# Optimization experiments

Measured on AMD Instinct MI355X. Metric: run time of the kernel, lower is better.

## Reference

```python
import jax, jax.numpy as jnp
import numpy as np

B, S, H = 2, 2048, 2048
INTER = 1024
N_ROUTED = 8
ZERO = 4
TOTAL = N_ROUTED + ZERO
TOP_K = 2
SCALE = 1.5


def setup_inputs() -> dict:
    key = jax.random.key(0)
    k0, k1, k2, k3, k4, k5 = jax.random.split(key, 6)
    w = 0.02  # weight init scale
    return {
        "hidden_states": jax.random.normal(k0, (B, S, H), jnp.float32),
        "classifier_w": jax.random.normal(k1, (TOTAL, H), jnp.float32) * w,
        "e_score_correction_bias": jax.random.normal(k2, (TOTAL,), jnp.float32) * w,
        "gate_w": jax.random.normal(k3, (N_ROUTED, INTER, H), jnp.float32) * w,
        "up_w": jax.random.normal(k4, (N_ROUTED, INTER, H), jnp.float32) * w,
        "down_w": jax.random.normal(k5, (N_ROUTED, H, INTER), jnp.float32) * w,
    }


def reference(hidden_states, classifier_w, e_score_correction_bias, gate_w, up_w, down_w):
    x = hidden_states  # [B,S,H]
    total = classifier_w.shape[0]
    n_routed = gate_w.shape[0]

    # --- Router: softmax over all experts, bias only for selection ---
    logits = jnp.einsum('bsh,eh->bse', x, classifier_w)          # [B,S,total]
    probs = jax.nn.softmax(logits, axis=-1)
    biased = probs + e_score_correction_bias
    _, idx = jax.lax.top_k(biased, TOP_K)                         # [B,S,K] int
    rw = jnp.take_along_axis(probs, idx, axis=-1) * SCALE         # unbiased probs as weights

    # Dense per-expert weight via one-hot combine (Equal+Mul+ReduceSum in original)
    w_full = jnp.sum(jax.nn.one_hot(idx, total, dtype=x.dtype) * rw[..., None], axis=-2)  # [B,S,total]

    # --- Compute ALL routed experts densely (matches original op graph) ---
    g = jnp.einsum('bsh,eih->bsei', x, gate_w)                    # [B,S,E,INTER]
    u = jnp.einsum('bsh,eih->bsei', x, up_w)
    act = jax.nn.silu(g) * u
    expert_out = jnp.einsum('bsei,ehi->bseh', act, down_w)        # [B,S,E,H]

    out = jnp.einsum('bse,bseh->bsh', w_full[..., :n_routed], expert_out)
    # Zero (identity) experts pass hidden_states through
    out = out + x * jnp.sum(w_full[..., n_routed:], axis=-1, keepdims=True)
    return out
```

## Files before the change

kernel.cpp:

```cpp
#include <hip/hip_runtime.h>
#include <cstdint>

#define T_TOKENS 4096
#define HDIM 2048
#define IDIM 1024
#define NEXP 8
#define NTOT 12
#define MAX_SLOTS 8320

typedef __bf16 bf16x8_t __attribute__((ext_vector_type(8)));
typedef float f32x4_t __attribute__((ext_vector_type(4)));
typedef unsigned short u16x8_t __attribute__((ext_vector_type(8)));
typedef unsigned short u16x4_t __attribute__((ext_vector_type(4)));

__device__ __forceinline__ unsigned short f2bf(float f) {
    unsigned int u = __builtin_bit_cast(unsigned int, f);
    u += 0x7fffu + ((u >> 16) & 1u);
    return (unsigned short)(u >> 16);
}
__device__ __forceinline__ float bfu2f(unsigned short u) {
    unsigned int v = ((unsigned int)u) << 16;
    return __builtin_bit_cast(float, v);
}
__device__ __forceinline__ void async16(const unsigned short* g, unsigned short* l) {
    __builtin_amdgcn_global_load_lds(
        (const unsigned int __attribute__((address_space(1)))*)g,
        (unsigned int __attribute__((address_space(3)))*)l,
        16, 0, 0);
}
__device__ __forceinline__ void cvt16(const float* src, unsigned short* dst) {
    f32x4_t f0 = ((const f32x4_t*)src)[0];
    f32x4_t f1 = ((const f32x4_t*)src)[1];
    f32x4_t f2 = ((const f32x4_t*)src)[2];
    f32x4_t f3 = ((const f32x4_t*)src)[3];
    u16x8_t a, b;
#pragma unroll
    for (int j = 0; j < 4; ++j) { a[j] = f2bf(f0[j]); a[4 + j] = f2bf(f1[j]); }
#pragma unroll
    for (int j = 0; j < 4; ++j) { b[j] = f2bf(f2[j]); b[4 + j] = f2bf(f3[j]); }
    ((u16x8_t*)dst)[0] = a;
    ((u16x8_t*)dst)[1] = b;
}

__global__ void init_kernel(int* __restrict__ meta) {
    int i = threadIdx.x;
    if (i < 32) meta[i] = 0;
}

__global__ void noop_kernel() {}

__global__ void cvtbf_kernel(const float* __restrict__ s, unsigned short* __restrict__ d, int n8) {
    int stride = gridDim.x * blockDim.x;
    for (int i = blockIdx.x * blockDim.x + threadIdx.x; i < n8; i += stride) {
        const f32x4_t* p = (const f32x4_t*)(s + (size_t)i * 8);
        f32x4_t a = p[0], b = p[1];
        u16x8_t o;
#pragma unroll
        for (int j = 0; j < 4; ++j) { o[j] = f2bf(a[j]); o[4 + j] = f2bf(b[j]); }
        ((u16x8_t*)d)[i] = o;
    }
}

__global__ void router_kernel(const float* __restrict__ x,
                              const float* __restrict__ cw,
                              const float* __restrict__ bias,
                              int* __restrict__ counts,
                              int* __restrict__ tok_e,
                              float* __restrict__ tok_w,
                              float* __restrict__ zero_w,
                              unsigned short* __restrict__ xb) {
    const int token = blockIdx.x;
    const int ln = threadIdx.x;
    const float* xr = x + (size_t)token * HDIM;
    float acc[NTOT];
#pragma unroll
    for (int e = 0; e < NTOT; ++e) acc[e] = 0.f;
    for (int h0 = ln * 4; h0 < HDIM; h0 += 256) {
        f32x4_t xv = *(const f32x4_t*)(xr + h0);
        if (xb) {
            u16x4_t o;
#pragma unroll
            for (int j = 0; j < 4; ++j) o[j] = f2bf(xv[j]);
            *(u16x4_t*)(xb + (size_t)token * HDIM + h0) = o;
        }
#pragma unroll
        for (int e = 0; e < NTOT; ++e) {
            f32x4_t wv = *(const f32x4_t*)(cw + e * HDIM + h0);
            acc[e] += xv[0] * wv[0] + xv[1] * wv[1] + xv[2] * wv[2] + xv[3] * wv[3];
        }
    }
#pragma unroll
    for (int e = 0; e < NTOT; ++e) {
        float v = acc[e];
#pragma unroll
        for (int s = 32; s > 0; s >>= 1) v += __shfl_xor(v, s, 64);
        acc[e] = v;
    }
    if (ln == 0) {
        float mx = acc[0];
#pragma unroll
        for (int e = 1; e < NTOT; ++e) mx = fmaxf(mx, acc[e]);
        float p[NTOT];
        float sum = 0.f;
#pragma unroll
        for (int e = 0; e < NTOT; ++e) { p[e] = __expf(acc[e] - mx); sum += p[e]; }
        float inv = 1.f / sum;
#pragma unroll
        for (int e = 0; e < NTOT; ++e) p[e] *= inv;
        float b[NTOT];
#pragma unroll
        for (int e = 0; e < NTOT; ++e) b[e] = p[e] + bias[e];
        int i0 = 0; float v0 = b[0];
#pragma unroll
        for (int e = 1; e < NTOT; ++e) if (b[e] > v0) { v0 = b[e]; i0 = e; }
        int i1 = -1; float v1 = -3.0e38f;
#pragma unroll
        for (int e = 0; e < NTOT; ++e) if (e != i0 && b[e] > v1) { v1 = b[e]; i1 = e; }
        if (i1 < 0) i1 = (i0 == 0) ? 1 : 0;
        float w0 = p[i0] * 1.5f, w1 = p[i1] * 1.5f;
        tok_e[2 * token] = i0; tok_e[2 * token + 1] = i1;
        tok_w[2 * token] = w0; tok_w[2 * token + 1] = w1;
        float zw = 0.f;
        if (i0 >= NEXP) zw += w0; else atomicAdd(&counts[i0], 1);
        if (i1 >= NEXP) zw += w1; else atomicAdd(&counts[i1], 1);
        zero_w[token] = zw;
    }
}

__global__ void scan_kernel(const int* __restrict__ counts, int* __restrict__ offs) {
    if (threadIdx.x == 0 && blockIdx.x == 0) {
        int a = 0;
        for (int e = 0; e < NEXP; ++e) {
            offs[e] = a;
            int c = counts[e];
            if (c < 0) c = 0;
            if (c > T_TOKENS) c = T_TOKENS;
            a += c;
        }
        if (a > 2 * T_TOKENS) a = 2 * T_TOKENS;
        offs[NEXP] = a;
    }
}

__global__ void place_kernel(const int* __restrict__ tok_e, const float* __restrict__ tok_w,
                             const int* __restrict__ offs, int* __restrict__ fill,
                             int* __restrict__ token_list, float* __restrict__ slot_w,
                             int* __restrict__ map) {
    int token = blockIdx.x * blockDim.x + threadIdx.x;
    if (token >= T_TOKENS) return;
#pragma unroll
    for (int j = 0; j < 2; ++j) {
        int e = tok_e[2 * token + j];
        int m = -1;
        if (e >= 0 && e < NEXP) {
            int pos = atomicAdd(&fill[e], 1);
            int slot = offs[e] + pos;
            if (slot >= 0 && slot < 2 * T_TOKENS) {
                token_list[slot] = token;
                slot_w[slot] = tok_w[2 * token + j];
                m = slot;
            }
        }
        map[2 * token + j] = m;
    }
}

__launch_bounds__(256, 3)
__global__ void gemm1_kernel(const unsigned short* __restrict__ xb,
                             const unsigned short* __restrict__ gwb,
                             const unsigned short* __restrict__ uwb,
                             const int* __restrict__ offs,
                             const int* __restrict__ token_list,
                             const float* __restrict__ slot_w,
                             unsigned short* __restrict__ act) {
    const int e = blockIdx.z;
    const int off = offs[e];
    int Me = offs[e + 1] - off;
    if (Me < 0) Me = 0;
    if (Me > T_TOKENS) Me = T_TOKENS;
    const int m0 = blockIdx.y * 64;
    if (m0 >= Me) return;
    const int n0 = blockIdx.x * 128;

    __shared__ __align__(16) unsigned short As[64][32];
    __shared__ __align__(16) unsigned short Gs[128][32];
    __shared__ __align__(16) unsigned short Us[128][32];

    const int tid = threadIdx.x;
    const int wv = tid >> 6, ln = tid & 63;

    int tr = m0 + wv * 16 + (ln >> 2);
    if (tr >= Me) tr = Me - 1;
    int tok = token_list[off + tr];
    if (tok < 0 || tok >= T_TOKENS) tok = 0;
    const unsigned short* aA = xb + (size_t)tok * HDIM + (ln & 3) * 8;
    unsigned short* lA = &As[wv * 16][0];

    const size_t wrow = (size_t)(n0 + wv * 32 + (ln >> 2)) * HDIM + (ln & 3) * 8;
    const unsigned short* aG0 = gwb + (size_t)e * IDIM * HDIM + wrow;
    const unsigned short* aG1 = aG0 + (size_t)16 * HDIM;
    const unsigned short* aU0 = uwb + (size_t)e * IDIM * HDIM + wrow;
    const unsigned short* aU1 = aU0 + (size_t)16 * HDIM;
    unsigned short* lG0 = &Gs[wv * 32][0];
    unsigned short* lG1 = &Gs[wv * 32 + 16][0];
    unsigned short* lU0 = &Us[wv * 32][0];
    unsigned short* lU1 = &Us[wv * 32 + 16][0];

    const int wm = wv & 1, wn = wv >> 1;
    const int fr = ln & 15;
    const int fk = (ln >> 4) * 8;

    f32x4_t accg[2][4] = {};
    f32x4_t accu[2][4] = {};

    for (int k0 = 0; k0 < HDIM; k0 += 32) {
        async16(aA + k0, lA);
        async16(aG0 + k0, lG0);
        async16(aG1 + k0, lG1);
        async16(aU0 + k0, lU0);
        async16(aU1 + k0, lU1);
        __syncthreads();
        bf16x8_t af[2], gf[4], uf[4];
#pragma unroll
        for (int t = 0; t < 2; ++t)
            af[t] = *(const bf16x8_t*)&As[wm * 32 + t * 16 + fr][fk];
#pragma unroll
        for (int t = 0; t < 4; ++t) {
            gf[t] = *(const bf16x8_t*)&Gs[wn * 64 + t * 16 + fr][fk];
            uf[t] = *(const bf16x8_t*)&Us[wn * 64 + t * 16 + fr][fk];
        }
#pragma unroll
        for (int mt = 0; mt < 2; ++mt)
#pragma unroll
            for (int nt = 0; nt < 4; ++nt) {
                accg[mt][nt] = __builtin_amdgcn_mfma_f32_16x16x32_bf16(af[mt], gf[nt], accg[mt][nt], 0, 0, 0);
                accu[mt][nt] = __builtin_amdgcn_mfma_f32_16x16x32_bf16(af[mt], uf[nt], accu[mt][nt], 0, 0, 0);
            }
        __syncthreads();
    }

#pragma unroll
    for (int mt = 0; mt < 2; ++mt) {
#pragma unroll
        for (int r = 0; r < 4; ++r) {
            int rloc = wm * 32 + mt * 16 + (ln >> 4) * 4 + r;
            int grow = m0 + rloc;
            if (grow < Me) {
                float w = slot_w[off + grow];
                size_t rb = (size_t)(off + grow) * IDIM + n0;
#pragma unroll
                for (int nt = 0; nt < 4; ++nt) {
                    float g = accg[mt][nt][r];
                    float u = accu[mt][nt][r];
                    float s = g / (1.f + __expf(-g));
                    act[rb + wn * 64 + nt * 16 + fr] = f2bf(s * u * w);
                }
            }
        }
    }
}

__launch_bounds__(256, 3)
__global__ void gemm2_kernel(const unsigned short* __restrict__ act,
                             const unsigned short* __restrict__ dwb,
                             const int* __restrict__ offs,
                             unsigned short* __restrict__ dout) {
    const int e = blockIdx.z;
    const int off = offs[e];
    int Me = offs[e + 1] - off;
    if (Me < 0) Me = 0;
    if (Me > T_TOKENS) Me = T_TOKENS;
    const int m0 = blockIdx.y * 128;
    if (m0 >= Me) return;
    const int n0 = blockIdx.x * 128;

    __shared__ __align__(16) unsigned short As[128][32];
    __shared__ __align__(16) unsigned short Bs[128][32];

    const int tid = threadIdx.x;
    const int wv = tid >> 6, ln = tid & 63;
    const int sc = (ln & 3) * 8;

    const int sr = wv * 16 + (ln >> 2);
    int ar0 = off + m0 + sr;      if (ar0 >= MAX_SLOTS) ar0 = MAX_SLOTS - 1;
    int ar1 = off + m0 + 64 + sr; if (ar1 >= MAX_SLOTS) ar1 = MAX_SLOTS - 1;
    const unsigned short* aA0 = act + (size_t)ar0 * IDIM + sc;
    const unsigned short* aA1 = act + (size_t)ar1 * IDIM + sc;
    unsigned short* lA0 = &As[wv * 16][0];
    unsigned short* lA1 = &As[64 + wv * 16][0];

    const unsigned short* aB0 = dwb + (size_t)e * HDIM * IDIM +
                                (size_t)(n0 + wv * 32 + (ln >> 2)) * IDIM + sc;
    const unsigned short* aB1 = aB0 + (size_t)16 * IDIM;
    unsigned short* lB0 = &Bs[wv * 32][0];
    unsigned short* lB1 = &Bs[wv * 32 + 16][0];

    const int wm = wv & 1, wn = wv >> 1;
    const int fr = ln & 15;
    const int fk = (ln >> 4) * 8;

    f32x4_t acc[4][4] = {};

    for (int k0 = 0; k0 < IDIM; k0 += 32) {
        async16(aA0 + k0, lA0);
        async16(aA1 + k0, lA1);
        async16(aB0 + k0, lB0);
        async16(aB1 + k0, lB1);
        __syncthreads();
        bf16x8_t af[4], bfr[4];
#pragma unroll
        for (int t = 0; t < 4; ++t) {
            af[t] = *(const bf16x8_t*)&As[wm * 64 + t * 16 + fr][fk];
            bfr[t] = *(const bf16x8_t*)&Bs[wn * 64 + t * 16 + fr][fk];
        }
#pragma unroll
        for (int mt = 0; mt < 4; ++mt)
#pragma unroll
            for (int nt = 0; nt < 4; ++nt)
                acc[mt][nt] = __builtin_amdgcn_mfma_f32_16x16x32_bf16(af[mt], bfr[nt], acc[mt][nt], 0, 0, 0);
        __syncthreads();
    }

#pragma unroll
    for (int mt = 0; mt < 4; ++mt) {
#pragma unroll
        for (int r = 0; r < 4; ++r) {
            int rloc = wm * 64 + mt * 16 + (ln >> 4) * 4 + r;
            int grow = m0 + rloc;
            if (grow < Me) {
                size_t rb = (size_t)(off + grow) * HDIM + n0;
#pragma unroll
                for (int nt = 0; nt < 4; ++nt)
                    dout[rb + wn * 64 + nt * 16 + fr] = f2bf(acc[mt][nt][r]);
            }
        }
    }
}

__launch_bounds__(256, 2)
__global__ void gemm1_fb(const float* __restrict__ x,
                         const float* __restrict__ gate_w,
                         const float* __restrict__ up_w,
                         const int* __restrict__ offs,
                         const int* __restrict__ token_list,
                         const float* __restrict__ slot_w,
                         unsigned short* __restrict__ act) {
    const int e = blockIdx.z;
    const int off = offs[e];
    int Me = offs[e + 1] - off;
    if (Me < 0) Me = 0;
    if (Me > T_TOKENS) Me = T_TOKENS;
    const int m0 = blockIdx.y * 128;
    if (m0 >= Me) return;
    const int n0 = blockIdx.x * 128;

    __shared__ __align__(16) unsigned short As[128][32];
    __shared__ __align__(16) unsigned short Gs[128][32];
    __shared__ __align__(16) unsigned short Us[128][32];

    const int tid = threadIdx.x;
    const int srow = tid >> 1;
    const int shalf = (tid & 1) * 16;

    int tr = m0 + srow; if (tr >= Me) tr = Me - 1;
    int tok = token_list[off + tr];
    if (tok < 0 || tok >= T_TOKENS) tok = 0;
    const float* aA = x + (size_t)tok * HDIM + shalf;
    const float* aG = gate_w + (size_t)e * IDIM * HDIM + (size_t)(n0 + srow) * HDIM + shalf;
    const float* aU = up_w + (size_t)e * IDIM * HDIM + (size_t)(n0 + srow) * HDIM + shalf;
    unsigned short* lA = &As[srow][shalf];
    unsigned short* lG = &Gs[srow][shalf];
    unsigned short* lU = &Us[srow][shalf];

    const int wv = tid >> 6, ln = tid & 63;
    const int wm = wv & 1, wn = wv >> 1;
    const int fr = ln & 15;
    const int fk = (ln >> 4) * 8;

    f32x4_t accg[4][4] = {};
    f32x4_t accu[4][4] = {};

    for (int k0 = 0; k0 < HDIM; k0 += 32) {
        cvt16(aA + k0, lA);
        cvt16(aG + k0, lG);
        cvt16(aU + k0, lU);
        __syncthreads();
        bf16x8_t af[4], gf[4], uf[4];
#pragma unroll
        for (int t = 0; t < 4; ++t) {
            af[t] = *(const bf16x8_t*)&As[wm * 64 + t * 16 + fr][fk];
            gf[t] = *(const bf16x8_t*)&Gs[wn * 64 + t * 16 + fr][fk];
            uf[t] = *(const bf16x8_t*)&Us[wn * 64 + t * 16 + fr][fk];
        }
#pragma unroll
        for (int mt = 0; mt < 4; ++mt)
#pragma unroll
            for (int nt = 0; nt < 4; ++nt) {
                accg[mt][nt] = __builtin_amdgcn_mfma_f32_16x16x32_bf16(af[mt], gf[nt], accg[mt][nt], 0, 0, 0);
                accu[mt][nt] = __builtin_amdgcn_mfma_f32_16x16x32_bf16(af[mt], uf[nt], accu[mt][nt], 0, 0, 0);
            }
        __syncthreads();
    }

#pragma unroll
    for (int mt = 0; mt < 4; ++mt) {
#pragma unroll
        for (int r = 0; r < 4; ++r) {
            int rloc = wm * 64 + mt * 16 + (ln >> 4) * 4 + r;
            int grow = m0 + rloc;
            if (grow < Me) {
                float w = slot_w[off + grow];
                size_t rb = (size_t)(off + grow) * IDIM + n0;
#pragma unroll
                for (int nt = 0; nt < 4; ++nt) {
                    float g = accg[mt][nt][r];
                    float u = accu[mt][nt][r];
                    float s = g / (1.f + __expf(-g));
                    act[rb + wn * 64 + nt * 16 + fr] = f2bf(s * u * w);
                }
            }
        }
    }
}

__launch_bounds__(256, 2)
__global__ void gemm2_fb(const unsigned short* __restrict__ act,
                         const float* __restrict__ dwn,
                         const int* __restrict__ offs,
                         unsigned short* __restrict__ dout) {
    const int e = blockIdx.z;
    const int off = offs[e];
    int Me = offs[e + 1] - off;
    if (Me < 0) Me = 0;
    if (Me > T_TOKENS) Me = T_TOKENS;
    const int m0 = blockIdx.y * 128;
    if (m0 >= Me) return;
    const int n0 = blockIdx.x * 128;

    __shared__ __align__(16) unsigned short As[128][32];
    __shared__ __align__(16) unsigned short Bs[128][32];

    const int tid = threadIdx.x;
    const int wv = tid >> 6, ln = tid & 63;

    const int sr0 = wv * 16 + (ln >> 2);
    const int sc = (ln & 3) * 8;
    int ar0 = off + m0 + sr0;      if (ar0 >= MAX_SLOTS) ar0 = MAX_SLOTS - 1;
    int ar1 = off + m0 + 64 + sr0; if (ar1 >= MAX_SLOTS) ar1 = MAX_SLOTS - 1;
    const unsigned short* aA0 = act + (size_t)ar0 * IDIM + sc;
    const unsigned short* aA1 = act + (size_t)ar1 * IDIM + sc;
    unsigned short* lA0 = &As[wv * 16][0];
    unsigned short* lA1 = &As[64 + wv * 16][0];

    const int srow = tid >> 1;
    const int shalf = (tid & 1) * 16;
    const float* aB = dwn + (size_t)e * HDIM * IDIM + (size_t)(n0 + srow) * IDIM + shalf;
    unsigned short* lB = &Bs[srow][shalf];

    const int wm = wv & 1, wn = wv >> 1;
    const int fr = ln & 15;
    const int fk = (ln >> 4) * 8;

    f32x4_t acc[4][4] = {};

    for (int k0 = 0; k0 < IDIM; k0 += 32) {
        async16(aA0 + k0, lA0);
        async16(aA1 + k0, lA1);
        cvt16(aB + k0, lB);
        __syncthreads();
        bf16x8_t af[4], bfr[4];
#pragma unroll
        for (int t = 0; t < 4; ++t) {
            af[t] = *(const bf16x8_t*)&As[wm * 64 + t * 16 + fr][fk];
            bfr[t] = *(const bf16x8_t*)&Bs[wn * 64 + t * 16 + fr][fk];
        }
#pragma unroll
        for (int mt = 0; mt < 4; ++mt)
#pragma unroll
            for (int nt = 0; nt < 4; ++nt)
                acc[mt][nt] = __builtin_amdgcn_mfma_f32_16x16x32_bf16(af[mt], bfr[nt], acc[mt][nt], 0, 0, 0);
        __syncthreads();
    }

#pragma unroll
    for (int mt = 0; mt < 4; ++mt) {
#pragma unroll
        for (int r = 0; r < 4; ++r) {
            int rloc = wm * 64 + mt * 16 + (ln >> 4) * 4 + r;
            int grow = m0 + rloc;
            if (grow < Me) {
                size_t rb = (size_t)(off + grow) * HDIM + n0;
#pragma unroll
                for (int nt = 0; nt < 4; ++nt)
                    dout[rb + wn * 64 + nt * 16 + fr] = f2bf(acc[mt][nt][r]);
            }
        }
    }
}

__global__ void finalize_kernel(const float* __restrict__ x,
                                const unsigned short* __restrict__ dout,
                                const int* __restrict__ map,
                                const float* __restrict__ zero_w,
                                float* __restrict__ out) {
    int gid = blockIdx.x * blockDim.x + threadIdx.x;
    int token = gid >> 8;
    int hg = (gid & 255) * 8;
    int s0 = map[2 * token], s1 = map[2 * token + 1];
    float zw = zero_w[token];
    size_t base = (size_t)token * HDIM + hg;
    f32x4_t x0 = *(const f32x4_t*)(x + base);
    f32x4_t x1 = *(const f32x4_t*)(x + base + 4);
    float o[8];
#pragma unroll
    for (int j = 0; j < 4; ++j) { o[j] = zw * x0[j]; o[4 + j] = zw * x1[j]; }
    if (s0 >= 0 && s0 < 2 * T_TOKENS) {
        u16x8_t d = *(const u16x8_t*)(dout + (size_t)s0 * HDIM + hg);
#pragma unroll
        for (int j = 0; j < 8; ++j) o[j] += bfu2f(d[j]);
    }
    if (s1 >= 0 && s1 < 2 * T_TOKENS) {
        u16x8_t d = *(const u16x8_t*)(dout + (size_t)s1 * HDIM + hg);
#pragma unroll
        for (int j = 0; j < 8; ++j) o[j] += bfu2f(d[j]);
    }
    f32x4_t o0, o1;
#pragma unroll
    for (int j = 0; j < 4; ++j) { o0[j] = o[j]; o1[j] = o[4 + j]; }
    *(f32x4_t*)(out + base) = o0;
    *(f32x4_t*)(out + base + 4) = o1;
}

extern "C" void kernel_launch(void* const* d_in, const int* in_sizes, int n_in,
                              void* d_out, int out_size, void* d_ws, size_t ws_size,
                              hipStream_t stream) {
    const float* x = (const float*)d_in[0];
    const float* cw = (const float*)d_in[1];
    const float* bias = (const float*)d_in[2];
    const float* gw = (const float*)d_in[3];
    const float* uw = (const float*)d_in[4];
    const float* dw = (const float*)d_in[5];
    float* out = (float*)d_out;

    char* ws = (char*)d_ws;
    int* counts = (int*)(ws + 0);
    int* fill = (int*)(ws + 32);
    int* offs = (int*)(ws + 64);
    int* tok_e = (int*)(ws + 128);
    float* tok_w = (float*)(ws + 32896);
    float* zero_w = (float*)(ws + 65664);
    int* map = (int*)(ws + 82048);
    int* token_list = (int*)(ws + 114816);
    float* slot_w = (float*)(ws + 148096);
    unsigned short* act = (unsigned short*)(ws + 181504);
    unsigned short* dout = (unsigned short*)(ws + 17220864);
    const size_t needed_small = 51299584ull;
    unsigned short* xb  = (unsigned short*)(ws + 51299584ull);
    unsigned short* gwb = (unsigned short*)(ws + 68076800ull);
    unsigned short* uwb = (unsigned short*)(ws + 101631232ull);
    unsigned short* dwb = (unsigned short*)(ws + 135185664ull);
    const size_t needed_big = 168740096ull;

    if (ws_size < needed_small) {
        noop_kernel<<<1, 64, 0, stream>>>();
        return;
    }

    init_kernel<<<1, 64, 0, stream>>>((int*)ws);

    if (ws_size >= needed_big) {
        router_kernel<<<T_TOKENS, 64, 0, stream>>>(x, cw, bias, counts, tok_e, tok_w, zero_w, xb);
        scan_kernel<<<1, 64, 0, stream>>>(counts, offs);
        place_kernel<<<(T_TOKENS + 255) / 256, 256, 0, stream>>>(tok_e, tok_w, offs, fill,
                                                                 token_list, slot_w, map);
        const int n8w = NEXP * IDIM * HDIM / 8;
        cvtbf_kernel<<<2048, 256, 0, stream>>>(gw, gwb, n8w);
        cvtbf_kernel<<<2048, 256, 0, stream>>>(uw, uwb, n8w);
        cvtbf_kernel<<<2048, 256, 0, stream>>>(dw, dwb, n8w);
        gemm1_kernel<<<dim3(IDIM / 128, 64, NEXP), 256, 0, stream>>>(xb, gwb, uwb, offs,
                                                                     token_list, slot_w, act);
        gemm2_kernel<<<dim3(HDIM / 128, 32, NEXP), 256, 0, stream>>>(act, dwb, offs, dout);
    } else {
        router_kernel<<<T_TOKENS, 64, 0, stream>>>(x, cw, bias, counts, tok_e, tok_w, zero_w,
                                                   (unsigned short*)nullptr);
        scan_kernel<<<1, 64, 0, stream>>>(counts, offs);
        place_kernel<<<(T_TOKENS + 255) / 256, 256, 0, stream>>>(tok_e, tok_w, offs, fill,
                                                                 token_list, slot_w, map);
        gemm1_fb<<<dim3(IDIM / 128, 32, NEXP), 256, 0, stream>>>(x, gw, uw, offs,
                                                                 token_list, slot_w, act);
        gemm2_fb<<<dim3(HDIM / 128, 32, NEXP), 256, 0, stream>>>(act, dw, offs, dout);
    }

    finalize_kernel<<<(T_TOKENS * HDIM / 8 + 255) / 256, 256, 0, stream>>>(x, dout, map,
                                                                           zero_w, out);
}
```

Baseline: 531.8 us.

## Interleave gate/up weights into one packed matrix and use 128x128 gemm1 tiles

Gate and up weights are converted to bf16 into one interleaved buffer: each 32-row block holds 16 gate rows followed by 16 up rows. This lets gemm1 run as a single 128x128 tile GEMM whose adjacent accumulator tiles pair gate with up for the SiLU epilogue. The three conversion kernels are merged into one launch, and the gemm2 B-tile row mapping is changed to contiguous 16-row chunks per wave. The aim is more MMA work per loaded A tile and fewer launches, at the cost of a scattered read pattern in the pack kernel and a larger accumulator register footprint in gemm1.

```diff
diff --git a/kernel.cpp b/kernel.cpp
--- a/kernel.cpp
+++ b/kernel.cpp
@@ -49,15 +49,37 @@
 
 __global__ void noop_kernel() {}
 
-__global__ void cvtbf_kernel(const float* __restrict__ s, unsigned short* __restrict__ d, int n8) {
+__global__ void pack_w_kernel(const float* __restrict__ gw, const float* __restrict__ uw,
+                              const float* __restrict__ dw,
+                              unsigned short* __restrict__ guwb,
+                              unsigned short* __restrict__ dwb) {
+    const int n8_gu = NEXP * 2 * IDIM * HDIM / 8;
+    const int n8_d = NEXP * HDIM * IDIM / 8;
     int stride = gridDim.x * blockDim.x;
-    for (int i = blockIdx.x * blockDim.x + threadIdx.x; i < n8; i += stride) {
-        const f32x4_t* p = (const f32x4_t*)(s + (size_t)i * 8);
-        f32x4_t a = p[0], b = p[1];
-        u16x8_t o;
-#pragma unroll
-        for (int j = 0; j < 4; ++j) { o[j] = f2bf(a[j]); o[4 + j] = f2bf(b[j]); }
-        ((u16x8_t*)d)[i] = o;
+    for (int i = blockIdx.x * blockDim.x + threadIdx.x; i < n8_gu + n8_d; i += stride) {
+        if (i < n8_gu) {
+            size_t f = (size_t)i * 8;
+            int h = (int)(f & (HDIM - 1));
+            int p = (int)((f >> 11) & 2047);
+            int e = (int)(f >> 22);
+            int j = p >> 5, r = p & 31;
+            const float* base = (r < 16) ? gw : uw;
+            const float* src = base + ((size_t)e * IDIM + 16 * j + (r & 15)) * HDIM + h;
+            f32x4_t a = ((const f32x4_t*)src)[0];
+            f32x4_t b = ((const f32x4_t*)src)[1];
+            u16x8_t o;
+#pragma unroll
+            for (int q = 0; q < 4; ++q) { o[q] = f2bf(a[q]); o[4 + q] = f2bf(b[q]); }
+            ((u16x8_t*)guwb)[i] = o;
+        } else {
+            int k = i - n8_gu;
+            const f32x4_t* p4 = (const f32x4_t*)(dw + (size_t)k * 8);
+            f32x4_t a = p4[0], b = p4[1];
+            u16x8_t o;
+#pragma unroll
+            for (int q = 0; q < 4; ++q) { o[q] = f2bf(a[q]); o[4 + q] = f2bf(b[q]); }
+            ((u16x8_t*)dwb)[k] = o;
+        }
     }
 }
 
@@ -167,8 +189,7 @@
 
 __launch_bounds__(256, 3)
 __global__ void gemm1_kernel(const unsigned short* __restrict__ xb,
-                             const unsigned short* __restrict__ gwb,
-                             const unsigned short* __restrict__ uwb,
+                             const unsigned short* __restrict__ guwb,
                              const int* __restrict__ offs,
                              const int* __restrict__ token_list,
                              const float* __restrict__ slot_w,
@@ -178,82 +199,74 @@
     int Me = offs[e + 1] - off;
     if (Me < 0) Me = 0;
     if (Me > T_TOKENS) Me = T_TOKENS;
-    const int m0 = blockIdx.y * 64;
+    const int m0 = blockIdx.y * 128;
     if (m0 >= Me) return;
     const int n0 = blockIdx.x * 128;
 
-    __shared__ __align__(16) unsigned short As[64][32];
-    __shared__ __align__(16) unsigned short Gs[128][32];
-    __shared__ __align__(16) unsigned short Us[128][32];
+    __shared__ __align__(16) unsigned short As[128][32];
+    __shared__ __align__(16) unsigned short Bs[128][32];
 
     const int tid = threadIdx.x;
     const int wv = tid >> 6, ln = tid & 63;
-
-    int tr = m0 + wv * 16 + (ln >> 2);
-    if (tr >= Me) tr = Me - 1;
-    int tok = token_list[off + tr];
-    if (tok < 0 || tok >= T_TOKENS) tok = 0;
-    const unsigned short* aA = xb + (size_t)tok * HDIM + (ln & 3) * 8;
-    unsigned short* lA = &As[wv * 16][0];
-
-    const size_t wrow = (size_t)(n0 + wv * 32 + (ln >> 2)) * HDIM + (ln & 3) * 8;
-    const unsigned short* aG0 = gwb + (size_t)e * IDIM * HDIM + wrow;
-    const unsigned short* aG1 = aG0 + (size_t)16 * HDIM;
-    const unsigned short* aU0 = uwb + (size_t)e * IDIM * HDIM + wrow;
-    const unsigned short* aU1 = aU0 + (size_t)16 * HDIM;
-    unsigned short* lG0 = &Gs[wv * 32][0];
-    unsigned short* lG1 = &Gs[wv * 32 + 16][0];
-    unsigned short* lU0 = &Us[wv * 32][0];
-    unsigned short* lU1 = &Us[wv * 32 + 16][0];
+    const int sc = (ln & 3) * 8;
+
+    int tr0 = m0 + wv * 16 + (ln >> 2);      if (tr0 >= Me) tr0 = Me - 1;
+    int tr1 = m0 + 64 + wv * 16 + (ln >> 2); if (tr1 >= Me) tr1 = Me - 1;
+    int tok0 = token_list[off + tr0]; if (tok0 < 0 || tok0 >= T_TOKENS) tok0 = 0;
+    int tok1 = token_list[off + tr1]; if (tok1 < 0 || tok1 >= T_TOKENS) tok1 = 0;
+    const unsigned short* aA0 = xb + (size_t)tok0 * HDIM + sc;
+    const unsigned short* aA1 = xb + (size_t)tok1 * HDIM + sc;
+    unsigned short* lA0 = &As[wv * 16][0];
+    unsigned short* lA1 = &As[64 + wv * 16][0];
+
+    const unsigned short* aB0 = guwb + (size_t)e * 2 * IDIM * HDIM +
+                                (size_t)(n0 + wv * 16 + (ln >> 2)) * HDIM + sc;
+    const unsigned short* aB1 = aB0 + (size_t)64 * HDIM;
+    unsigned short* lB0 = &Bs[wv * 16][0];
+    unsigned short* lB1 = &Bs[64 + wv * 16][0];
 
     const int wm = wv & 1, wn = wv >> 1;
     const int fr = ln & 15;
     const int fk = (ln >> 4) * 8;
 
-    f32x4_t accg[2][4] = {};
-    f32x4_t accu[2][4] = {};
+    f32x4_t acc[4][4] = {};
 
     for (int k0 = 0; k0 < HDIM; k0 += 32) {
-        async16(aA + k0, lA);
-        async16(aG0 + k0, lG0);
-        async16(aG1 + k0, lG1);
-        async16(aU0 + k0, lU0);
-        async16(aU1 + k0, lU1);
-        __syncthreads();
-        bf16x8_t af[2], gf[4], uf[4];
-#pragma unroll
-        for (int t = 0; t < 2; ++t)
-            af[t] = *(const bf16x8_t*)&As[wm * 32 + t * 16 + fr][fk];
+        async16(aA0 + k0, lA0);
+        async16(aA1 + k0, lA1);
+        async16(aB0 + k0, lB0);
+        async16(aB1 + k0, lB1);
+        __syncthreads();
+        bf16x8_t af[4], bfr[4];
 #pragma unroll
         for (int t = 0; t < 4; ++t) {
-            gf[t] = *(const bf16x8_t*)&Gs[wn * 64 + t * 16 + fr][fk];
-            uf[t] = *(const bf16x8_t*)&Us[wn * 64 + t * 16 + fr][fk];
-        }
-#pragma unroll
-        for (int mt = 0; mt < 2; ++mt)
-#pragma unroll
-            for (int nt = 0; nt < 4; ++nt) {
-                accg[mt][nt] = __builtin_amdgcn_mfma_f32_16x16x32_bf16(af[mt], gf[nt], accg[mt][nt], 0, 0, 0);
-                accu[mt][nt] = __builtin_amdgcn_mfma_f32_16x16x32_bf16(af[mt], uf[nt], accu[mt][nt], 0, 0, 0);
-            }
-        __syncthreads();
-    }
-
-#pragma unroll
-    for (int mt = 0; mt < 2; ++mt) {
+            af[t] = *(const bf16x8_t*)&As[wm * 64 + t * 16 + fr][fk];
+            bfr[t] = *(const bf16x8_t*)&Bs[wn * 64 + t * 16 + fr][fk];
+        }
+#pragma unroll
+        for (int mt = 0; mt < 4; ++mt)
+#pragma unroll
+            for (int nt = 0; nt < 4; ++nt)
+                acc[mt][nt] = __builtin_amdgcn_mfma_f32_16x16x32_bf16(af[mt], bfr[nt], acc[mt][nt], 0, 0, 0);
+        __syncthreads();
+    }
+
+    const int ibase = (n0 >> 1) + wn * 32;
+#pragma unroll
+    for (int mt = 0; mt < 4; ++mt) {
 #pragma unroll
         for (int r = 0; r < 4; ++r) {
-            int rloc = wm * 32 + mt * 16 + (ln >> 4) * 4 + r;
+            int rloc = wm * 64 + mt * 16 + (ln >> 4) * 4 + r;
             int grow = m0 + rloc;
             if (grow < Me) {
                 float w = slot_w[off + grow];
-                size_t rb = (size_t)(off + grow) * IDIM + n0;
-#pragma unroll
-                for (int nt = 0; nt < 4; ++nt) {
-                    float g = accg[mt][nt][r];
-                    float u = accu[mt][nt][r];
+                size_t rb = (size_t)(off + grow) * IDIM + ibase;
+#pragma unroll
+                for (int t = 0; t < 2; ++t) {
+                    float g = acc[mt][2 * t][r];
+                    float u = acc[mt][2 * t + 1][r];
                     float s = g / (1.f + __expf(-g));
-                    act[rb + wn * 64 + nt * 16 + fr] = f2bf(s * u * w);
+                    act[rb + t * 16 + fr] = f2bf(s * u * w);
                 }
             }
         }
@@ -290,10 +303,10 @@
     unsigned short* lA1 = &As[64 + wv * 16][0];
 
     const unsigned short* aB0 = dwb + (size_t)e * HDIM * IDIM +
-                                (size_t)(n0 + wv * 32 + (ln >> 2)) * IDIM + sc;
-    const unsigned short* aB1 = aB0 + (size_t)16 * IDIM;
-    unsigned short* lB0 = &Bs[wv * 32][0];
-    unsigned short* lB1 = &Bs[wv * 32 + 16][0];
+                                (size_t)(n0 + wv * 16 + (ln >> 2)) * IDIM + sc;
+    const unsigned short* aB1 = aB0 + (size_t)64 * IDIM;
+    unsigned short* lB0 = &Bs[wv * 16][0];
+    unsigned short* lB1 = &Bs[64 + wv * 16][0];
 
     const int wm = wv & 1, wn = wv >> 1;
     const int fr = ln & 15;
@@ -555,10 +568,9 @@
     unsigned short* act = (unsigned short*)(ws + 181504);
     unsigned short* dout = (unsigned short*)(ws + 17220864);
     const size_t needed_small = 51299584ull;
-    unsigned short* xb  = (unsigned short*)(ws + 51299584ull);
-    unsigned short* gwb = (unsigned short*)(ws + 68076800ull);
-    unsigned short* uwb = (unsigned short*)(ws + 101631232ull);
-    unsigned short* dwb = (unsigned short*)(ws + 135185664ull);
+    unsigned short* xb   = (unsigned short*)(ws + 51299584ull);
+    unsigned short* guwb = (unsigned short*)(ws + 68076800ull);
+    unsigned short* dwb  = (unsigned short*)(ws + 135185664ull);
     const size_t needed_big = 168740096ull;
 
     if (ws_size < needed_small) {
@@ -573,12 +585,9 @@
         scan_kernel<<<1, 64, 0, stream>>>(counts, offs);
         place_kernel<<<(T_TOKENS + 255) / 256, 256, 0, stream>>>(tok_e, tok_w, offs, fill,
                                                                  token_list, slot_w, map);
-        const int n8w = NEXP * IDIM * HDIM / 8;
-        cvtbf_kernel<<<2048, 256, 0, stream>>>(gw, gwb, n8w);
-        cvtbf_kernel<<<2048, 256, 0, stream>>>(uw, uwb, n8w);
-        cvtbf_kernel<<<2048, 256, 0, stream>>>(dw, dwb, n8w);
-        gemm1_kernel<<<dim3(IDIM / 128, 64, NEXP), 256, 0, stream>>>(xb, gwb, uwb, offs,
-                                                                     token_list, slot_w, act);
+        pack_w_kernel<<<4096, 256, 0, stream>>>(gw, uw, dw, guwb, dwb);
+        gemm1_kernel<<<dim3(2 * IDIM / 128, 32, NEXP), 256, 0, stream>>>(xb, guwb, offs,
+                                                                         token_list, slot_w, act);
         gemm2_kernel<<<dim3(HDIM / 128, 32, NEXP), 256, 0, stream>>>(act, dwb, offs, dout);
     } else {
         router_kernel<<<T_TOKENS, 64, 0, stream>>>(x, cw, bias, counts, tok_e, tok_w, zero_w,
```

Result: faster. 500.4 us (-5.9%).
